# Performance work log

Hardware: AMD Instinct MI355X
Metric: run time of the kernel (lower is better)

## Reference

```python
import jax, jax.numpy as jnp
import numpy as np

B = 1_000_000
NG = 4          # distance_embed_dim -> 4x0e scalars per edge feature
MAX_OFF = 5.0   # max_cross_offset (GaussianSmearing stop)

# e3nn FullyConnectedTensorProduct path coefficients:
#   coeff = sqrt(dim(ir_out) / fan_in_elements) * w3j_entry
# where w3j entries are 1 (000), 1/sqrt(3) (011/101/110), eps/sqrt(6) (111).
# tp1: irreps (4x0e+1e) x (4x0e+1e) -> 20x0e + 5x1e
#   fan_in(0e) = 4*4 + 1*1 = 17 ; fan_in(1e) = 4*1 + 1*4 + 1*1 = 9
C1_000 = (1.0 / 17.0) ** 0.5
C1_110 = (1.0 / 17.0) ** 0.5 / 3.0 ** 0.5
C1_011 = (3.0 / 9.0) ** 0.5 / 3.0 ** 0.5
C1_101 = C1_011
C1_111 = (3.0 / 9.0) ** 0.5 / 6.0 ** 0.5
# tp2: (20x0e+5x1e) x (4x0e+1e) -> 9x0e + 1x1e
#   fan_in(0e) = 20*4 + 5*1 = 85 ; fan_in(1e) = 20*1 + 5*4 + 5*1 = 45
C2_000 = (1.0 / 85.0) ** 0.5
C2_110 = (1.0 / 85.0) ** 0.5 / 3.0 ** 0.5
C2_011 = (3.0 / 45.0) ** 0.5 / 3.0 ** 0.5
C2_101 = C2_011
C2_111 = (3.0 / 45.0) ** 0.5 / 6.0 ** 0.5


def setup_inputs() -> dict:
    key = jax.random.key(0)
    ks = jax.random.split(key, 12)
    f32 = jnp.float32
    return dict(
        ligand=jax.random.normal(ks[0], (B, 4, 3), f32),
        receptor=jax.random.normal(ks[1], (B, 4, 3), f32) + 1.0,
        # tp1 weights (mul-1 axes squeezed): paths 000,110,011,101,111
        w1_000=jax.random.normal(ks[2], (NG, NG, 20), f32),
        w1_110=jax.random.normal(ks[3], (20,), f32),
        w1_011=jax.random.normal(ks[4], (NG, 5), f32),
        w1_101=jax.random.normal(ks[5], (NG, 5), f32),
        w1_111=jax.random.normal(ks[6], (5,), f32),
        # tp2 weights
        w2_000=jax.random.normal(ks[7], (20, NG, 9), f32),
        w2_110=jax.random.normal(ks[8], (5, 9), f32),
        w2_011=jax.random.normal(ks[9], (20,), f32),
        w2_101=jax.random.normal(ks[10], (5, NG), f32),
        w2_111=jax.random.normal(ks[11], (5,), f32),
    )


def _forward(ligand, receptor, w1_000, w1_110, w1_011, w1_101, w1_111,
             w2_000, w2_110, w2_011, w2_101, w2_111):
    edge_vec = ligand - receptor                                 # (B,4,3)
    dist = jnp.sqrt(jnp.sum(edge_vec * edge_vec, -1, keepdims=True))  # (B,4,1)
    offset = jnp.linspace(0.0, MAX_OFF, NG).astype(ligand.dtype)  # (NG,)
    coeff = -0.5 / (offset[1] - offset[0]) ** 2
    emb = jnp.exp(coeff * (dist - offset) ** 2)                  # (B,4,NG)
    unit = edge_vec / dist                                       # (B,4,3)
    s1, v1 = emb[:, 1], unit[:, 1]
    s2, v2 = emb[:, 2], unit[:, 2]
    s3, v3 = emb[:, 3], unit[:, 3]
    # ---- tp1: (s1,v1) x (s2,v2) -> S (B,20), V (B,5,3) ----
    dot12 = jnp.sum(v1 * v2, -1)                                 # (B,)
    S = (C1_000 * jnp.einsum('uvw,bu,bv->bw', w1_000, s1, s2)
         + C1_110 * dot12[:, None] * w1_110)
    cr12 = jnp.cross(v1, v2)                                     # (B,3)
    V = (C1_011 * jnp.einsum('uw,bu,bk->bwk', w1_011, s1, v2)
         + C1_101 * jnp.einsum('vw,bv,bk->bwk', w1_101, s2, v1)
         + C1_111 * w1_111[None, :, None] * cr12[:, None, :])
    # ---- tp2: (S,V) x (s3,v3) -> out (B,12) = 9x0e + 1x1e ----
    Vd3 = jnp.einsum('buk,bk->bu', V, v3)                        # (B,5)
    S2 = (C2_000 * jnp.einsum('uvw,bu,bv->bw', w2_000, S, s3)
          + C2_110 * jnp.einsum('uw,bu->bw', w2_110, Vd3))
    Vx3 = jnp.cross(V, v3[:, None, :])                           # (B,5,3)
    V2 = (C2_011 * jnp.einsum('u,bu,bk->bk', w2_011, S, v3)
          + C2_101 * jnp.einsum('uv,buk,bv->bk', w2_101, V, s3)
          + C2_111 * jnp.einsum('u,buk->bk', w2_111, Vx3))
    return jnp.concatenate([S2, V2], -1)                         # (B,12)


def reference(ligand, receptor, w1_000, w1_110, w1_011, w1_101, w1_111,
              w2_000, w2_110, w2_011, w2_101, w2_111):
    out = _forward(ligand, receptor, w1_000, w1_110, w1_011, w1_101, w1_111,
                   w2_000, w2_110, w2_011, w2_101, w2_111)
    s_rot, s_tr = out[:, :3], out[:, 3:6]
    t_rot, t_tr = out[:, 6:9], out[:, 9:12]
    return s_rot, s_tr, t_rot, t_tr
```

## Files before the change

### kernel.cpp

```cpp
#include <hip/hip_runtime.h>
#include <math.h>


#define K_A   (0.10846522890932808f * 0.24253562503633297f)
#define K_B   (0.10846522890932808f * 0.14002800840979312f)
#define K_P   (0.06262242910851495f * 0.33333333333333333f)
#define K_Q   (0.06262242910851495f * 0.33333333333333333f)
#define K_R   (0.06262242910851495f * 0.23570226039551584f)
#define K_WB  (0.14907119849998599f * 0.24253562503633297f)
#define K_CB  (0.14907119849998599f * 0.14002800840979312f)
#define K_WA  (0.14907119849998599f * 0.33333333333333333f)
#define K_WBT (0.14907119849998599f * 0.33333333333333333f)
#define K_WC  (0.14907119849998599f * 0.23570226039551584f)
#define K_WA3 (0.10540925533894598f * 0.33333333333333333f)
#define K_WB3 (0.10540925533894598f * 0.33333333333333333f)
#define K_WC3 (0.10540925533894598f * 0.23570226039551584f)

#define EX_WB   720
#define EX_CB   736
#define EX_WA   740
#define EX_WBT  756
#define EX_WC   772
#define EX_WA3  776
#define EX_WB3  780
#define EX_WC3  784
#define N_WS    785

__global__ void fd8_prep(const float* __restrict__ w1_000, const float* __restrict__ w1_110,
                         const float* __restrict__ w1_011, const float* __restrict__ w1_101,
                         const float* __restrict__ w1_111, const float* __restrict__ w2_000,
                         const float* __restrict__ w2_110, const float* __restrict__ w2_011,
                         const float* __restrict__ w2_101, const float* __restrict__ w2_111,
                         float* __restrict__ ws)
{
    int j = threadIdx.x;
    if (j >= N_WS) return;
    float val = 0.f;
    if (j < 720) {
        int r = j / 9, c = j - r * 9;
        if (r < 64) {
            int pq = r >> 2, v = r & 3;
            float a = 0.f;
            for (int u = 0; u < 20; ++u)
                a = fmaf(w1_000[pq * 20 + u], w2_000[u * 36 + v * 9 + c], a);
            val = K_A * a;
        } else if (r < 68) {
            int v = r - 64; float a = 0.f;
            for (int u = 0; u < 20; ++u)
                a = fmaf(w1_110[u], w2_000[u * 36 + v * 9 + c], a);
            val = K_B * a;
        } else if (r < 72) {
            int u = r - 68; float a = 0.f;
            for (int m = 0; m < 5; ++m)
                a = fmaf(w1_011[u * 5 + m], w2_110[m * 9 + c], a);
            val = K_P * a;
        } else if (r < 76) {
            int u = r - 72; float a = 0.f;
            for (int m = 0; m < 5; ++m)
                a = fmaf(w1_101[u * 5 + m], w2_110[m * 9 + c], a);
            val = K_Q * a;
        } else if (r == 76) {
            float a = 0.f;
            for (int m = 0; m < 5; ++m)
                a = fmaf(w1_111[m], w2_110[m * 9 + c], a);
            val = K_R * a;
        }
    } else {
        int k = j - 720;
        if (k < 16) {
            float a = 0.f;
            for (int u = 0; u < 20; ++u)
                a = fmaf(w2_011[u], w1_000[k * 20 + u], a);
            val = K_WB * a;
        } else if (k == 16) {
            float a = 0.f;
            for (int u = 0; u < 20; ++u)
                a = fmaf(w2_011[u], w1_110[u], a);
            val = K_CB * a;
        } else if (k >= 20 && k < 36) {
            int u = (k - 20) >> 2, v = (k - 20) & 3;
            float a = 0.f;
            for (int m = 0; m < 5; ++m)
                a = fmaf(w1_011[u * 5 + m], w2_101[m * 4 + v], a);
            val = K_WA * a;
        } else if (k >= 36 && k < 52) {
            int u = (k - 36) >> 2, v = (k - 36) & 3;
            float a = 0.f;
            for (int m = 0; m < 5; ++m)
                a = fmaf(w1_101[u * 5 + m], w2_101[m * 4 + v], a);
            val = K_WBT * a;
        } else if (k >= 52 && k < 56) {
            int v = k - 52; float a = 0.f;
            for (int m = 0; m < 5; ++m)
                a = fmaf(w1_111[m], w2_101[m * 4 + v], a);
            val = K_WC * a;
        } else if (k >= 56 && k < 60) {
            int u = k - 56; float a = 0.f;
            for (int m = 0; m < 5; ++m)
                a = fmaf(w2_111[m], w1_011[u * 5 + m], a);
            val = K_WA3 * a;
        } else if (k >= 60 && k < 64) {
            int v = k - 60; float a = 0.f;
            for (int m = 0; m < 5; ++m)
                a = fmaf(w2_111[m], w1_101[v * 5 + m], a);
            val = K_WB3 * a;
        } else if (k == 64) {
            float a = 0.f;
            for (int m = 0; m < 5; ++m)
                a = fmaf(w2_111[m], w1_111[m], a);
            val = K_WC3 * a;
        }
    }
    ws[j] = val;
}

__global__ __launch_bounds__(256) void
fd8(const float* __restrict__ lig, const float* __restrict__ rec,
    const float* __restrict__ ws, float* __restrict__ out, int n)
{
    const int tid = blockIdx.x * 256 + threadIdx.x;
    if (tid >= n) return;

    const float4* L = (const float4*)(lig + (size_t)tid * 12);
    const float4* R = (const float4*)(rec + (size_t)tid * 12);
    float4 l0 = L[0], l1 = L[1], l2 = L[2];
    float4 r0 = R[0], r1 = R[1], r2 = R[2];

    float e1x = l0.w - r0.w, e1y = l1.x - r1.x, e1z = l1.y - r1.y;
    float e2x = l1.z - r1.z, e2y = l1.w - r1.w, e2z = l2.x - r2.x;
    float e3x = l2.y - r2.y, e3y = l2.z - r2.z, e3z = l2.w - r2.w;

    float n1 = fmaf(e1x, e1x, fmaf(e1y, e1y, e1z * e1z));
    float n2 = fmaf(e2x, e2x, fmaf(e2y, e2y, e2z * e2z));
    float n3sq = fmaf(e3x, e3x, fmaf(e3y, e3y, e3z * e3z));
    float i1 = __builtin_amdgcn_rsqf(n1);
    float i2 = __builtin_amdgcn_rsqf(n2);
    float i3 = __builtin_amdgcn_rsqf(n3sq);
    float d1 = n1 * i1, d2 = n2 * i2, d3 = n3sq * i3;

    float v1x = e1x * i1, v1y = e1y * i1, v1z = e1z * i1;
    float v2x = e2x * i2, v2y = e2y * i2, v2z = e2z * i2;
    float v3x = e3x * i3, v3y = e3y * i3, v3z = e3z * i3;

    const float coeff = -0.18f;
    const float o1 = 1.6666666f, o2 = 3.3333333f, o3 = 5.f;
    float s1[4], s2[4], s3[4];
    float x;
    x = d1;      s1[0] = __expf(coeff * x * x);
    x = d1 - o1; s1[1] = __expf(coeff * x * x);
    x = d1 - o2; s1[2] = __expf(coeff * x * x);
    x = d1 - o3; s1[3] = __expf(coeff * x * x);
    x = d2;      s2[0] = __expf(coeff * x * x);
    x = d2 - o1; s2[1] = __expf(coeff * x * x);
    x = d2 - o2; s2[2] = __expf(coeff * x * x);
    x = d2 - o3; s2[3] = __expf(coeff * x * x);
    x = d3;      s3[0] = __expf(coeff * x * x);
    x = d3 - o1; s3[1] = __expf(coeff * x * x);
    x = d3 - o2; s3[2] = __expf(coeff * x * x);
    x = d3 - o3; s3[3] = __expf(coeff * x * x);

    float dot12 = v1x * v2x + v1y * v2y + v1z * v2z;
    float d13   = v1x * v3x + v1y * v3y + v1z * v3z;
    float d23   = v2x * v3x + v2y * v3y + v2z * v3z;
    float c12x = v1y * v2z - v1z * v2y;
    float c12y = v1z * v2x - v1x * v2z;
    float c12z = v1x * v2y - v1y * v2x;
    float dtp  = c12x * v3x + c12y * v3y + c12z * v3z;

    float acc0 = 0.f, acc1 = 0.f, acc2 = 0.f, acc3 = 0.f, acc4 = 0.f;
    float acc5 = 0.f, acc6 = 0.f, acc7 = 0.f, acc8 = 0.f;

#define GROUP4(g, x0v, x1v, x2v, x3v) do { \
    const float* wp_ = ws + 36 * (g); \
    const float x0_ = (x0v), x1_ = (x1v), x2_ = (x2v), x3_ = (x3v); \
    acc0 = fmaf(x0_, wp_[0], acc0);  acc1 = fmaf(x0_, wp_[1], acc1); \
    acc2 = fmaf(x0_, wp_[2], acc2);  acc3 = fmaf(x0_, wp_[3], acc3); \
    acc4 = fmaf(x0_, wp_[4], acc4);  acc5 = fmaf(x0_, wp_[5], acc5); \
    acc6 = fmaf(x0_, wp_[6], acc6);  acc7 = fmaf(x0_, wp_[7], acc7); \
    acc8 = fmaf(x0_, wp_[8], acc8); \
    acc0 = fmaf(x1_, wp_[9], acc0);  acc1 = fmaf(x1_, wp_[10], acc1); \
    acc2 = fmaf(x1_, wp_[11], acc2); acc3 = fmaf(x1_, wp_[12], acc3); \
    acc4 = fmaf(x1_, wp_[13], acc4); acc5 = fmaf(x1_, wp_[14], acc5); \
    acc6 = fmaf(x1_, wp_[15], acc6); acc7 = fmaf(x1_, wp_[16], acc7); \
    acc8 = fmaf(x1_, wp_[17], acc8); \
    acc0 = fmaf(x2_, wp_[18], acc0); acc1 = fmaf(x2_, wp_[19], acc1); \
    acc2 = fmaf(x2_, wp_[20], acc2); acc3 = fmaf(x2_, wp_[21], acc3); \
    acc4 = fmaf(x2_, wp_[22], acc4); acc5 = fmaf(x2_, wp_[23], acc5); \
    acc6 = fmaf(x2_, wp_[24], acc6); acc7 = fmaf(x2_, wp_[25], acc7); \
    acc8 = fmaf(x2_, wp_[26], acc8); \
    acc0 = fmaf(x3_, wp_[27], acc0); acc1 = fmaf(x3_, wp_[28], acc1); \
    acc2 = fmaf(x3_, wp_[29], acc2); acc3 = fmaf(x3_, wp_[30], acc3); \
    acc4 = fmaf(x3_, wp_[31], acc4); acc5 = fmaf(x3_, wp_[32], acc5); \
    acc6 = fmaf(x3_, wp_[33], acc6); acc7 = fmaf(x3_, wp_[34], acc7); \
    acc8 = fmaf(x3_, wp_[35], acc8); \
} while (0)

    float sg = dot12 * ws[EX_CB];

#pragma unroll
    for (int p = 0; p < 4; ++p) {
#pragma unroll
        for (int q = 0; q < 4; ++q) {
            const int pq = p * 4 + q;
            float o = s1[p] * s2[q];
            sg = fmaf(o, ws[EX_WB + pq], sg);
            GROUP4(pq, o * s3[0], o * s3[1], o * s3[2], o * s3[3]);
        }
    }
    GROUP4(16, dot12 * s3[0], dot12 * s3[1], dot12 * s3[2], dot12 * s3[3]);
    GROUP4(17, d23 * s1[0], d23 * s1[1], d23 * s1[2], d23 * s1[3]);
    GROUP4(18, d13 * s2[0], d13 * s2[1], d13 * s2[2], d13 * s2[3]);
    {
        const float* wp = ws + 36 * 19;
        acc0 = fmaf(dtp, wp[0], acc0); acc1 = fmaf(dtp, wp[1], acc1);
        acc2 = fmaf(dtp, wp[2], acc2); acc3 = fmaf(dtp, wp[3], acc3);
        acc4 = fmaf(dtp, wp[4], acc4); acc5 = fmaf(dtp, wp[5], acc5);
        acc6 = fmaf(dtp, wp[6], acc6); acc7 = fmaf(dtp, wp[7], acc7);
        acc8 = fmaf(dtp, wp[8], acc8);
    }
#undef GROUP4

    float ta = 0.f, tb = 0.f;
#pragma unroll
    for (int u = 0; u < 4; ++u) {
        float da = fmaf(ws[EX_WA + u * 4 + 0], s3[0], fmaf(ws[EX_WA + u * 4 + 1], s3[1],
                   fmaf(ws[EX_WA + u * 4 + 2], s3[2], ws[EX_WA + u * 4 + 3] * s3[3])));
        float db = fmaf(ws[EX_WBT + u * 4 + 0], s3[0], fmaf(ws[EX_WBT + u * 4 + 1], s3[1],
                   fmaf(ws[EX_WBT + u * 4 + 2], s3[2], ws[EX_WBT + u * 4 + 3] * s3[3])));
        ta = fmaf(s1[u], da, ta);
        tb = fmaf(s2[u], db, tb);
    }
    float tc = fmaf(ws[EX_WC + 0], s3[0], fmaf(ws[EX_WC + 1], s3[1],
               fmaf(ws[EX_WC + 2], s3[2], ws[EX_WC + 3] * s3[3])));
    float wa = fmaf(ws[EX_WA3 + 0], s1[0], fmaf(ws[EX_WA3 + 1], s1[1],
               fmaf(ws[EX_WA3 + 2], s1[2], ws[EX_WA3 + 3] * s1[3])));
    float wb = fmaf(ws[EX_WB3 + 0], s2[0], fmaf(ws[EX_WB3 + 1], s2[1],
               fmaf(ws[EX_WB3 + 2], s2[2], ws[EX_WB3 + 3] * s2[3])));
    float wc = ws[EX_WC3];

    float c23x = v2y * v3z - v2z * v3y;
    float c23y = v2z * v3x - v2x * v3z;
    float c23z = v2x * v3y - v2y * v3x;
    float c13x = v1y * v3z - v1z * v3y;
    float c13y = v1z * v3x - v1x * v3z;
    float c13z = v1x * v3y - v1y * v3x;
    float ccrx = c12y * v3z - c12z * v3y;
    float ccry = c12z * v3x - c12x * v3z;
    float ccrz = c12x * v3y - c12y * v3x;

    float V2x = sg * v3x + ta * v2x + tb * v1x + tc * c12x + wa * c23x + wb * c13x + wc * ccrx;
    float V2y = sg * v3y + ta * v2y + tb * v1y + tc * c12y + wa * c23y + wb * c13y + wc * ccry;
    float V2z = sg * v3z + ta * v2z + tb * v1z + tc * c12z + wa * c23z + wb * c13z + wc * ccrz;

    const size_t n3 = (size_t)n * 3;
    const size_t base = (size_t)tid * 3;
    out[base + 0] = acc0;
    out[base + 1] = acc1;
    out[base + 2] = acc2;
    out[n3 + base + 0] = acc3;
    out[n3 + base + 1] = acc4;
    out[n3 + base + 2] = acc5;
    out[2 * n3 + base + 0] = acc6;
    out[2 * n3 + base + 1] = acc7;
    out[2 * n3 + base + 2] = acc8;
    out[3 * n3 + base + 0] = V2x;
    out[3 * n3 + base + 1] = V2y;
    out[3 * n3 + base + 2] = V2z;
}

extern "C" void kernel_launch(void* const* d_in, const int* in_sizes, int n_in,
                              void* d_out, int out_size, void* d_ws, size_t ws_size,
                              hipStream_t stream) {
    const float* lig = (const float*)d_in[0];
    const float* rec = (const float*)d_in[1];
    float* ws = (float*)d_ws;

    fd8_prep<<<1, 1024, 0, stream>>>(
        (const float*)d_in[2], (const float*)d_in[3], (const float*)d_in[4],
        (const float*)d_in[5], (const float*)d_in[6], (const float*)d_in[7],
        (const float*)d_in[8], (const float*)d_in[9], (const float*)d_in[10],
        (const float*)d_in[11], ws);

    int n = in_sizes[0] / 12;
    int blocks = (n + 255) / 256;
    fd8<<<blocks, 256, 0, stream>>>(lig, rec, ws, (float*)d_out, n);
}
```

Before: 162.6 us.

## Process two edges per thread to share weight loads and vectorize stores

Each thread now computes two consecutive batch elements, so every weight value read from the workspace feeds FMAs for both elements, halving scalar/L1 weight-load traffic per element. Output stores become float2 writes covering the pair. The prep kernel is split into 4 blocks of 256 threads. The cost is higher register pressure from doubled accumulators and half as many threads, which may reduce occupancy and latency hiding on a memory-bound kernel.

```diff
diff --git a/kernel.cpp b/kernel.cpp
--- a/kernel.cpp
+++ b/kernel.cpp
@@ -26,14 +26,14 @@
 #define EX_WC3  784
 #define N_WS    785
 
-__global__ void fd8_prep(const float* __restrict__ w1_000, const float* __restrict__ w1_110,
+__global__ void fd9_prep(const float* __restrict__ w1_000, const float* __restrict__ w1_110,
                          const float* __restrict__ w1_011, const float* __restrict__ w1_101,
                          const float* __restrict__ w1_111, const float* __restrict__ w2_000,
                          const float* __restrict__ w2_110, const float* __restrict__ w2_011,
                          const float* __restrict__ w2_101, const float* __restrict__ w2_111,
                          float* __restrict__ ws)
 {
-    int j = threadIdx.x;
+    int j = blockIdx.x * 256 + threadIdx.x;
     if (j >= N_WS) return;
     float val = 0.f;
     if (j < 720) {
@@ -115,157 +115,204 @@
 }
 
 __global__ __launch_bounds__(256) void
-fd8(const float* __restrict__ lig, const float* __restrict__ rec,
+fd9(const float* __restrict__ lig, const float* __restrict__ rec,
     const float* __restrict__ ws, float* __restrict__ out, int n)
 {
-    const int tid = blockIdx.x * 256 + threadIdx.x;
-    if (tid >= n) return;
-
-    const float4* L = (const float4*)(lig + (size_t)tid * 12);
-    const float4* R = (const float4*)(rec + (size_t)tid * 12);
-    float4 l0 = L[0], l1 = L[1], l2 = L[2];
-    float4 r0 = R[0], r1 = R[1], r2 = R[2];
-
-    float e1x = l0.w - r0.w, e1y = l1.x - r1.x, e1z = l1.y - r1.y;
-    float e2x = l1.z - r1.z, e2y = l1.w - r1.w, e2z = l2.x - r2.x;
-    float e3x = l2.y - r2.y, e3y = l2.z - r2.z, e3z = l2.w - r2.w;
-
-    float n1 = fmaf(e1x, e1x, fmaf(e1y, e1y, e1z * e1z));
-    float n2 = fmaf(e2x, e2x, fmaf(e2y, e2y, e2z * e2z));
-    float n3sq = fmaf(e3x, e3x, fmaf(e3y, e3y, e3z * e3z));
-    float i1 = __builtin_amdgcn_rsqf(n1);
-    float i2 = __builtin_amdgcn_rsqf(n2);
-    float i3 = __builtin_amdgcn_rsqf(n3sq);
-    float d1 = n1 * i1, d2 = n2 * i2, d3 = n3sq * i3;
-
-    float v1x = e1x * i1, v1y = e1y * i1, v1z = e1z * i1;
-    float v2x = e2x * i2, v2y = e2y * i2, v2z = e2z * i2;
-    float v3x = e3x * i3, v3y = e3y * i3, v3z = e3z * i3;
-
-    const float coeff = -0.18f;
-    const float o1 = 1.6666666f, o2 = 3.3333333f, o3 = 5.f;
-    float s1[4], s2[4], s3[4];
-    float x;
-    x = d1;      s1[0] = __expf(coeff * x * x);
-    x = d1 - o1; s1[1] = __expf(coeff * x * x);
-    x = d1 - o2; s1[2] = __expf(coeff * x * x);
-    x = d1 - o3; s1[3] = __expf(coeff * x * x);
-    x = d2;      s2[0] = __expf(coeff * x * x);
-    x = d2 - o1; s2[1] = __expf(coeff * x * x);
-    x = d2 - o2; s2[2] = __expf(coeff * x * x);
-    x = d2 - o3; s2[3] = __expf(coeff * x * x);
-    x = d3;      s3[0] = __expf(coeff * x * x);
-    x = d3 - o1; s3[1] = __expf(coeff * x * x);
-    x = d3 - o2; s3[2] = __expf(coeff * x * x);
-    x = d3 - o3; s3[3] = __expf(coeff * x * x);
-
-    float dot12 = v1x * v2x + v1y * v2y + v1z * v2z;
-    float d13   = v1x * v3x + v1y * v3y + v1z * v3z;
-    float d23   = v2x * v3x + v2y * v3y + v2z * v3z;
-    float c12x = v1y * v2z - v1z * v2y;
-    float c12y = v1z * v2x - v1x * v2z;
-    float c12z = v1x * v2y - v1y * v2x;
-    float dtp  = c12x * v3x + c12y * v3y + c12z * v3z;
-
-    float acc0 = 0.f, acc1 = 0.f, acc2 = 0.f, acc3 = 0.f, acc4 = 0.f;
-    float acc5 = 0.f, acc6 = 0.f, acc7 = 0.f, acc8 = 0.f;
-
-#define GROUP4(g, x0v, x1v, x2v, x3v) do { \
+    const int t = blockIdx.x * 256 + threadIdx.x;
+    const size_t iA = (size_t)t * 2;
+    if (iA >= (size_t)n) return;
+    const bool two = (iA + 1) < (size_t)n;
+    const size_t iB = two ? iA + 1 : iA;
+
+    float4 lA0, lA1, lA2, rA0, rA1, rA2, lB0, lB1, lB2, rB0, rB1, rB2;
+    {
+        const float4* LA = (const float4*)(lig + iA * 12);
+        const float4* RA = (const float4*)(rec + iA * 12);
+        const float4* LB = (const float4*)(lig + iB * 12);
+        const float4* RB = (const float4*)(rec + iB * 12);
+        lA0 = LA[0]; lA1 = LA[1]; lA2 = LA[2];
+        lB0 = LB[0]; lB1 = LB[1]; lB2 = LB[2];
+        rA0 = RA[0]; rA1 = RA[1]; rA2 = RA[2];
+        rB0 = RB[0]; rB1 = RB[1]; rB2 = RB[2];
+    }
+
+    float s1[2][4], s2[2][4], s3[2][4];
+    float v1[2][3], v2[2][3], v3[2][3], c12[2][3];
+    float dot12[2], d13[2], d23[2], dtp[2];
+
+#pragma unroll
+    for (int k = 0; k < 2; ++k) {
+        float4 l0 = k ? lB0 : lA0, l1 = k ? lB1 : lA1, l2 = k ? lB2 : lA2;
+        float4 r0 = k ? rB0 : rA0, r1 = k ? rB1 : rA1, r2 = k ? rB2 : rA2;
+
+        float e1x = l0.w - r0.w, e1y = l1.x - r1.x, e1z = l1.y - r1.y;
+        float e2x = l1.z - r1.z, e2y = l1.w - r1.w, e2z = l2.x - r2.x;
+        float e3x = l2.y - r2.y, e3y = l2.z - r2.z, e3z = l2.w - r2.w;
+
+        float n1 = fmaf(e1x, e1x, fmaf(e1y, e1y, e1z * e1z));
+        float n2 = fmaf(e2x, e2x, fmaf(e2y, e2y, e2z * e2z));
+        float n3q = fmaf(e3x, e3x, fmaf(e3y, e3y, e3z * e3z));
+        float i1 = __builtin_amdgcn_rsqf(n1);
+        float i2 = __builtin_amdgcn_rsqf(n2);
+        float i3 = __builtin_amdgcn_rsqf(n3q);
+        float d1 = n1 * i1, d2 = n2 * i2, d3 = n3q * i3;
+
+        v1[k][0] = e1x * i1; v1[k][1] = e1y * i1; v1[k][2] = e1z * i1;
+        v2[k][0] = e2x * i2; v2[k][1] = e2y * i2; v2[k][2] = e2z * i2;
+        v3[k][0] = e3x * i3; v3[k][1] = e3y * i3; v3[k][2] = e3z * i3;
+
+        const float coeff = -0.18f;
+        const float o1 = 1.6666666f, o2 = 3.3333333f, o3 = 5.f;
+        float x;
+        x = d1;      s1[k][0] = __expf(coeff * x * x);
+        x = d1 - o1; s1[k][1] = __expf(coeff * x * x);
+        x = d1 - o2; s1[k][2] = __expf(coeff * x * x);
+        x = d1 - o3; s1[k][3] = __expf(coeff * x * x);
+        x = d2;      s2[k][0] = __expf(coeff * x * x);
+        x = d2 - o1; s2[k][1] = __expf(coeff * x * x);
+        x = d2 - o2; s2[k][2] = __expf(coeff * x * x);
+        x = d2 - o3; s2[k][3] = __expf(coeff * x * x);
+        x = d3;      s3[k][0] = __expf(coeff * x * x);
+        x = d3 - o1; s3[k][1] = __expf(coeff * x * x);
+        x = d3 - o2; s3[k][2] = __expf(coeff * x * x);
+        x = d3 - o3; s3[k][3] = __expf(coeff * x * x);
+
+        dot12[k] = v1[k][0] * v2[k][0] + v1[k][1] * v2[k][1] + v1[k][2] * v2[k][2];
+        d13[k]   = v1[k][0] * v3[k][0] + v1[k][1] * v3[k][1] + v1[k][2] * v3[k][2];
+        d23[k]   = v2[k][0] * v3[k][0] + v2[k][1] * v3[k][1] + v2[k][2] * v3[k][2];
+        c12[k][0] = v1[k][1] * v2[k][2] - v1[k][2] * v2[k][1];
+        c12[k][1] = v1[k][2] * v2[k][0] - v1[k][0] * v2[k][2];
+        c12[k][2] = v1[k][0] * v2[k][1] - v1[k][1] * v2[k][0];
+        dtp[k] = c12[k][0] * v3[k][0] + c12[k][1] * v3[k][1] + c12[k][2] * v3[k][2];
+    }
+
+    float acc[2][9] = {{0.f,0.f,0.f,0.f,0.f,0.f,0.f,0.f,0.f},
+                       {0.f,0.f,0.f,0.f,0.f,0.f,0.f,0.f,0.f}};
+
+#define GROUP4(g, xa0, xa1, xa2, xa3, xb0, xb1, xb2, xb3) do { \
     const float* wp_ = ws + 36 * (g); \
-    const float x0_ = (x0v), x1_ = (x1v), x2_ = (x2v), x3_ = (x3v); \
-    acc0 = fmaf(x0_, wp_[0], acc0);  acc1 = fmaf(x0_, wp_[1], acc1); \
-    acc2 = fmaf(x0_, wp_[2], acc2);  acc3 = fmaf(x0_, wp_[3], acc3); \
-    acc4 = fmaf(x0_, wp_[4], acc4);  acc5 = fmaf(x0_, wp_[5], acc5); \
-    acc6 = fmaf(x0_, wp_[6], acc6);  acc7 = fmaf(x0_, wp_[7], acc7); \
-    acc8 = fmaf(x0_, wp_[8], acc8); \
-    acc0 = fmaf(x1_, wp_[9], acc0);  acc1 = fmaf(x1_, wp_[10], acc1); \
-    acc2 = fmaf(x1_, wp_[11], acc2); acc3 = fmaf(x1_, wp_[12], acc3); \
-    acc4 = fmaf(x1_, wp_[13], acc4); acc5 = fmaf(x1_, wp_[14], acc5); \
-    acc6 = fmaf(x1_, wp_[15], acc6); acc7 = fmaf(x1_, wp_[16], acc7); \
-    acc8 = fmaf(x1_, wp_[17], acc8); \
-    acc0 = fmaf(x2_, wp_[18], acc0); acc1 = fmaf(x2_, wp_[19], acc1); \
-    acc2 = fmaf(x2_, wp_[20], acc2); acc3 = fmaf(x2_, wp_[21], acc3); \
-    acc4 = fmaf(x2_, wp_[22], acc4); acc5 = fmaf(x2_, wp_[23], acc5); \
-    acc6 = fmaf(x2_, wp_[24], acc6); acc7 = fmaf(x2_, wp_[25], acc7); \
-    acc8 = fmaf(x2_, wp_[26], acc8); \
-    acc0 = fmaf(x3_, wp_[27], acc0); acc1 = fmaf(x3_, wp_[28], acc1); \
-    acc2 = fmaf(x3_, wp_[29], acc2); acc3 = fmaf(x3_, wp_[30], acc3); \
-    acc4 = fmaf(x3_, wp_[31], acc4); acc5 = fmaf(x3_, wp_[32], acc5); \
-    acc6 = fmaf(x3_, wp_[33], acc6); acc7 = fmaf(x3_, wp_[34], acc7); \
-    acc8 = fmaf(x3_, wp_[35], acc8); \
+    const float xa_[4] = { (xa0), (xa1), (xa2), (xa3) }; \
+    const float xb_[4] = { (xb0), (xb1), (xb2), (xb3) }; \
+    _Pragma("unroll") \
+    for (int r_ = 0; r_ < 4; ++r_) { \
+        _Pragma("unroll") \
+        for (int c_ = 0; c_ < 9; ++c_) { \
+            const float w_ = wp_[r_ * 9 + c_]; \
+            acc[0][c_] = fmaf(xa_[r_], w_, acc[0][c_]); \
+            acc[1][c_] = fmaf(xb_[r_], w_, acc[1][c_]); \
+        } \
+    } \
 } while (0)
 
-    float sg = dot12 * ws[EX_CB];
+    const float cb = ws[EX_CB];
+    float sg[2] = { dot12[0] * cb, dot12[1] * cb };
 
 #pragma unroll
     for (int p = 0; p < 4; ++p) {
 #pragma unroll
         for (int q = 0; q < 4; ++q) {
             const int pq = p * 4 + q;
-            float o = s1[p] * s2[q];
-            sg = fmaf(o, ws[EX_WB + pq], sg);
-            GROUP4(pq, o * s3[0], o * s3[1], o * s3[2], o * s3[3]);
-        }
-    }
-    GROUP4(16, dot12 * s3[0], dot12 * s3[1], dot12 * s3[2], dot12 * s3[3]);
-    GROUP4(17, d23 * s1[0], d23 * s1[1], d23 * s1[2], d23 * s1[3]);
-    GROUP4(18, d13 * s2[0], d13 * s2[1], d13 * s2[2], d13 * s2[3]);
+            const float oA = s1[0][p] * s2[0][q];
+            const float oB = s1[1][p] * s2[1][q];
+            const float wbq = ws[EX_WB + pq];
+            sg[0] = fmaf(oA, wbq, sg[0]);
+            sg[1] = fmaf(oB, wbq, sg[1]);
+            GROUP4(pq, oA * s3[0][0], oA * s3[0][1], oA * s3[0][2], oA * s3[0][3],
+                       oB * s3[1][0], oB * s3[1][1], oB * s3[1][2], oB * s3[1][3]);
+        }
+    }
+    GROUP4(16, dot12[0] * s3[0][0], dot12[0] * s3[0][1], dot12[0] * s3[0][2], dot12[0] * s3[0][3],
+               dot12[1] * s3[1][0], dot12[1] * s3[1][1], dot12[1] * s3[1][2], dot12[1] * s3[1][3]);
+    GROUP4(17, d23[0] * s1[0][0], d23[0] * s1[0][1], d23[0] * s1[0][2], d23[0] * s1[0][3],
+               d23[1] * s1[1][0], d23[1] * s1[1][1], d23[1] * s1[1][2], d23[1] * s1[1][3]);
+    GROUP4(18, d13[0] * s2[0][0], d13[0] * s2[0][1], d13[0] * s2[0][2], d13[0] * s2[0][3],
+               d13[1] * s2[1][0], d13[1] * s2[1][1], d13[1] * s2[1][2], d13[1] * s2[1][3]);
     {
         const float* wp = ws + 36 * 19;
-        acc0 = fmaf(dtp, wp[0], acc0); acc1 = fmaf(dtp, wp[1], acc1);
-        acc2 = fmaf(dtp, wp[2], acc2); acc3 = fmaf(dtp, wp[3], acc3);
-        acc4 = fmaf(dtp, wp[4], acc4); acc5 = fmaf(dtp, wp[5], acc5);
-        acc6 = fmaf(dtp, wp[6], acc6); acc7 = fmaf(dtp, wp[7], acc7);
-        acc8 = fmaf(dtp, wp[8], acc8);
+#pragma unroll
+        for (int c = 0; c < 9; ++c) {
+            acc[0][c] = fmaf(dtp[0], wp[c], acc[0][c]);
+            acc[1][c] = fmaf(dtp[1], wp[c], acc[1][c]);
+        }
     }
 #undef GROUP4
 
-    float ta = 0.f, tb = 0.f;
+    float ta[2] = {0.f, 0.f}, tb[2] = {0.f, 0.f};
 #pragma unroll
     for (int u = 0; u < 4; ++u) {
-        float da = fmaf(ws[EX_WA + u * 4 + 0], s3[0], fmaf(ws[EX_WA + u * 4 + 1], s3[1],
-                   fmaf(ws[EX_WA + u * 4 + 2], s3[2], ws[EX_WA + u * 4 + 3] * s3[3])));
-        float db = fmaf(ws[EX_WBT + u * 4 + 0], s3[0], fmaf(ws[EX_WBT + u * 4 + 1], s3[1],
-                   fmaf(ws[EX_WBT + u * 4 + 2], s3[2], ws[EX_WBT + u * 4 + 3] * s3[3])));
-        ta = fmaf(s1[u], da, ta);
-        tb = fmaf(s2[u], db, tb);
-    }
-    float tc = fmaf(ws[EX_WC + 0], s3[0], fmaf(ws[EX_WC + 1], s3[1],
-               fmaf(ws[EX_WC + 2], s3[2], ws[EX_WC + 3] * s3[3])));
-    float wa = fmaf(ws[EX_WA3 + 0], s1[0], fmaf(ws[EX_WA3 + 1], s1[1],
-               fmaf(ws[EX_WA3 + 2], s1[2], ws[EX_WA3 + 3] * s1[3])));
-    float wb = fmaf(ws[EX_WB3 + 0], s2[0], fmaf(ws[EX_WB3 + 1], s2[1],
-               fmaf(ws[EX_WB3 + 2], s2[2], ws[EX_WB3 + 3] * s2[3])));
-    float wc = ws[EX_WC3];
-
-    float c23x = v2y * v3z - v2z * v3y;
-    float c23y = v2z * v3x - v2x * v3z;
-    float c23z = v2x * v3y - v2y * v3x;
-    float c13x = v1y * v3z - v1z * v3y;
-    float c13y = v1z * v3x - v1x * v3z;
-    float c13z = v1x * v3y - v1y * v3x;
-    float ccrx = c12y * v3z - c12z * v3y;
-    float ccry = c12z * v3x - c12x * v3z;
-    float ccrz = c12x * v3y - c12y * v3x;
-
-    float V2x = sg * v3x + ta * v2x + tb * v1x + tc * c12x + wa * c23x + wb * c13x + wc * ccrx;
-    float V2y = sg * v3y + ta * v2y + tb * v1y + tc * c12y + wa * c23y + wb * c13y + wc * ccry;
-    float V2z = sg * v3z + ta * v2z + tb * v1z + tc * c12z + wa * c23z + wb * c13z + wc * ccrz;
+        const float a0 = ws[EX_WA + u * 4 + 0], a1 = ws[EX_WA + u * 4 + 1];
+        const float a2 = ws[EX_WA + u * 4 + 2], a3 = ws[EX_WA + u * 4 + 3];
+        const float b0 = ws[EX_WBT + u * 4 + 0], b1 = ws[EX_WBT + u * 4 + 1];
+        const float b2 = ws[EX_WBT + u * 4 + 2], b3 = ws[EX_WBT + u * 4 + 3];
+#pragma unroll
+        for (int k = 0; k < 2; ++k) {
+            float da = fmaf(a0, s3[k][0], fmaf(a1, s3[k][1], fmaf(a2, s3[k][2], a3 * s3[k][3])));
+            float db = fmaf(b0, s3[k][0], fmaf(b1, s3[k][1], fmaf(b2, s3[k][2], b3 * s3[k][3])));
+            ta[k] = fmaf(s1[k][u], da, ta[k]);
+            tb[k] = fmaf(s2[k][u], db, tb[k]);
+        }
+    }
+    const float wc = ws[EX_WC3];
+    float tc[2], wav[2], wbv[2];
+#pragma unroll
+    for (int k = 0; k < 2; ++k) {
+        tc[k]  = fmaf(ws[EX_WC + 0], s3[k][0], fmaf(ws[EX_WC + 1], s3[k][1],
+                 fmaf(ws[EX_WC + 2], s3[k][2], ws[EX_WC + 3] * s3[k][3])));
+        wav[k] = fmaf(ws[EX_WA3 + 0], s1[k][0], fmaf(ws[EX_WA3 + 1], s1[k][1],
+                 fmaf(ws[EX_WA3 + 2], s1[k][2], ws[EX_WA3 + 3] * s1[k][3])));
+        wbv[k] = fmaf(ws[EX_WB3 + 0], s2[k][0], fmaf(ws[EX_WB3 + 1], s2[k][1],
+                 fmaf(ws[EX_WB3 + 2], s2[k][2], ws[EX_WB3 + 3] * s2[k][3])));
+    }
+
+    float V2x[2], V2y[2], V2z[2];
+#pragma unroll
+    for (int k = 0; k < 2; ++k) {
+        float c23x = v2[k][1] * v3[k][2] - v2[k][2] * v3[k][1];
+        float c23y = v2[k][2] * v3[k][0] - v2[k][0] * v3[k][2];
+        float c23z = v2[k][0] * v3[k][1] - v2[k][1] * v3[k][0];
+        float c13x = v1[k][1] * v3[k][2] - v1[k][2] * v3[k][1];
+        float c13y = v1[k][2] * v3[k][0] - v1[k][0] * v3[k][2];
+        float c13z = v1[k][0] * v3[k][1] - v1[k][1] * v3[k][0];
+        float ccrx = c12[k][1] * v3[k][2] - c12[k][2] * v3[k][1];
+        float ccry = c12[k][2] * v3[k][0] - c12[k][0] * v3[k][2];
+        float ccrz = c12[k][0] * v3[k][1] - c12[k][1] * v3[k][0];
+        V2x[k] = sg[k] * v3[k][0] + ta[k] * v2[k][0] + tb[k] * v1[k][0]
+               + tc[k] * c12[k][0] + wav[k] * c23x + wbv[k] * c13x + wc * ccrx;
+        V2y[k] = sg[k] * v3[k][1] + ta[k] * v2[k][1] + tb[k] * v1[k][1]
+               + tc[k] * c12[k][1] + wav[k] * c23y + wbv[k] * c13y + wc * ccry;
+        V2z[k] = sg[k] * v3[k][2] + ta[k] * v2[k][2] + tb[k] * v1[k][2]
+               + tc[k] * c12[k][2] + wav[k] * c23z + wbv[k] * c13z + wc * ccrz;
+    }
 
     const size_t n3 = (size_t)n * 3;
-    const size_t base = (size_t)tid * 3;
-    out[base + 0] = acc0;
-    out[base + 1] = acc1;
-    out[base + 2] = acc2;
-    out[n3 + base + 0] = acc3;
-    out[n3 + base + 1] = acc4;
-    out[n3 + base + 2] = acc5;
-    out[2 * n3 + base + 0] = acc6;
-    out[2 * n3 + base + 1] = acc7;
-    out[2 * n3 + base + 2] = acc8;
-    out[3 * n3 + base + 0] = V2x;
-    out[3 * n3 + base + 1] = V2y;
-    out[3 * n3 + base + 2] = V2z;
+    const size_t base = iA * 3;
+    if (two) {
+        *(float2*)(out + base + 0)          = make_float2(acc[0][0], acc[0][1]);
+        *(float2*)(out + base + 2)          = make_float2(acc[0][2], acc[1][0]);
+        *(float2*)(out + base + 4)          = make_float2(acc[1][1], acc[1][2]);
+        *(float2*)(out + n3 + base + 0)     = make_float2(acc[0][3], acc[0][4]);
+        *(float2*)(out + n3 + base + 2)     = make_float2(acc[0][5], acc[1][3]);
+        *(float2*)(out + n3 + base + 4)     = make_float2(acc[1][4], acc[1][5]);
+        *(float2*)(out + 2 * n3 + base + 0) = make_float2(acc[0][6], acc[0][7]);
+        *(float2*)(out + 2 * n3 + base + 2) = make_float2(acc[0][8], acc[1][6]);
+        *(float2*)(out + 2 * n3 + base + 4) = make_float2(acc[1][7], acc[1][8]);
+        *(float2*)(out + 3 * n3 + base + 0) = make_float2(V2x[0], V2y[0]);
+        *(float2*)(out + 3 * n3 + base + 2) = make_float2(V2z[0], V2x[1]);
+        *(float2*)(out + 3 * n3 + base + 4) = make_float2(V2y[1], V2z[1]);
+    } else {
+        out[base + 0] = acc[0][0];
+        out[base + 1] = acc[0][1];
+        out[base + 2] = acc[0][2];
+        out[n3 + base + 0] = acc[0][3];
+        out[n3 + base + 1] = acc[0][4];
+        out[n3 + base + 2] = acc[0][5];
+        out[2 * n3 + base + 0] = acc[0][6];
+        out[2 * n3 + base + 1] = acc[0][7];
+        out[2 * n3 + base + 2] = acc[0][8];
+        out[3 * n3 + base + 0] = V2x[0];
+        out[3 * n3 + base + 1] = V2y[0];
+        out[3 * n3 + base + 2] = V2z[0];
+    }
 }
 
 extern "C" void kernel_launch(void* const* d_in, const int* in_sizes, int n_in,
@@ -275,13 +322,14 @@
     const float* rec = (const float*)d_in[1];
     float* ws = (float*)d_ws;
 
-    fd8_prep<<<1, 1024, 0, stream>>>(
+    fd9_prep<<<4, 256, 0, stream>>>(
         (const float*)d_in[2], (const float*)d_in[3], (const float*)d_in[4],
         (const float*)d_in[5], (const float*)d_in[6], (const float*)d_in[7],
         (const float*)d_in[8], (const float*)d_in[9], (const float*)d_in[10],
         (const float*)d_in[11], ws);
 
     int n = in_sizes[0] / 12;
-    int blocks = (n + 255) / 256;
-    fd8<<<blocks, 256, 0, stream>>>(lig, rec, ws, (float*)d_out, n);
+    int nPairs = (n + 1) / 2;
+    int blocks = (nPairs + 255) / 256;
+    fd9<<<blocks, 256, 0, stream>>>(lig, rec, ws, (float*)d_out, n);
 }
```

Result: slower. 218.5 us (+34.4%).
